# Kernel tuning notes

Hardware: AMD Instinct MI355X
Metric: run time of the kernel (lower is better)

Reference implementation:

```python
import jax, jax.numpy as jnp
import numpy as np

# --- dims (match init_kwargs) ---
H = 2048      # hidden_dim
NH = 16       # num_heads
QL = 1536     # q_latent_dim
KVL = 512     # kv_latent_dim
QR = 64       # q_rope_dim (== k_rope_dim)
QN = 128      # q_nope_dim
KR = 64       # k_rope_dim
KN = 128      # k_nope_dim
VD = 128      # v_dim
B, S = 1, 2048
BASE = 10000.0
EPS = 1e-6


def rms_norm(x, w, eps=EPS):
    xf = x.astype(jnp.float32)
    var = jnp.mean(xf * xf, axis=-1, keepdims=True)
    return w * (xf * jax.lax.rsqrt(var + eps)).astype(x.dtype)


def rope_cos_sin(seq_len, dim, base=BASE):
    inv_freq = 1.0 / (base ** (jnp.arange(0, dim, 2, dtype=jnp.float32) / dim))
    t = jnp.arange(seq_len, dtype=jnp.float32)
    freqs = jnp.outer(t, inv_freq)
    emb = jnp.concatenate([freqs, freqs], axis=-1)  # [S, dim]
    return jnp.cos(emb), jnp.sin(emb)


def rotate_half(x):
    d = x.shape[-1] // 2
    return jnp.concatenate([-x[..., d:], x[..., :d]], axis=-1)


def apply_rotary_pos_emb(q, k, cos, sin, position_ids):
    # cos/sin: [S, d]; position_ids: [B, S] -> [B, 1, S, d]
    cos = cos[position_ids][:, None]
    sin = sin[position_ids][:, None]

    def interleave(x):  # matches view(b,h,s,d//2,2).transpose(4,3).reshape
        b, h, s, d = x.shape
        return x.reshape(b, h, s, d // 2, 2).transpose(0, 1, 2, 4, 3).reshape(b, h, s, d)

    q = interleave(q)
    k = interleave(k)
    return q * cos + rotate_half(q) * sin, k * cos + rotate_half(k) * sin


def setup_inputs() -> dict:
    key = jax.random.key(0)
    ks = jax.random.split(key, 8)
    sc = 0.02
    hidden_states = jax.random.normal(ks[0], (B, S, H), dtype=jnp.float32)
    position_ids = jnp.broadcast_to(jnp.arange(S, dtype=jnp.int32), (B, S))
    attn_mask = jnp.tril(jnp.ones((S, S), dtype=jnp.int32))[None, None]  # causal, [1,1,S,S]
    return {
        "hidden_states": hidden_states,
        "position_ids": position_ids,
        "attn_mask": attn_mask,
        "q_down_w": jax.random.normal(ks[1], (QL, H), jnp.float32) * sc,
        "kv_down_w": jax.random.normal(ks[2], (KVL + KR, H), jnp.float32) * sc,
        "q_up_w": jax.random.normal(ks[3], (NH * (QN + QR), QL), jnp.float32) * sc,
        "k_up_w": jax.random.normal(ks[4], (NH * (KN + VD), KVL), jnp.float32) * sc,
        "o_w": jax.random.normal(ks[5], (H, NH * VD), jnp.float32) * sc,
        "q_norm_w": jnp.ones((QL,), jnp.float32),
        "kv_norm_w": jnp.ones((KVL + KR,), jnp.float32),
    }


def reference(hidden_states, position_ids, attn_mask, q_down_w, kv_down_w,
              q_up_w, k_up_w, o_w, q_norm_w, kv_norm_w):
    bsz, seq_len, _ = hidden_states.shape

    # --- query path: down-proj -> RMSNorm -> up-proj ---
    latent_cq = rms_norm(hidden_states @ q_down_w.T, q_norm_w)        # [B,S,QL]
    q = latent_cq @ q_up_w.T                                          # [B,S,NH*(QN+QR)]
    q = q.reshape(bsz, seq_len, NH, QN + QR).transpose(0, 2, 1, 3)    # [B,NH,S,QN+QR]
    q_nope, q_pe = q[..., :QN], q[..., QN:]

    # --- kv path: down-proj -> RMSNorm -> split latent / shared k_pe ---
    compressed_kv = rms_norm(hidden_states @ kv_down_w.T, kv_norm_w)  # [B,S,KVL+KR]
    latent_ckv, k_pe = compressed_kv[..., :KVL], compressed_kv[..., KVL:]
    kv = latent_ckv @ k_up_w.T                                        # [B,S,NH*(KN+VD)]
    kv = kv.reshape(bsz, seq_len, NH, KN + VD).transpose(0, 2, 1, 3)  # [B,NH,S,KN+VD]
    k_nope, value = kv[..., :KN], kv[..., KN:]

    # --- partial RoPE on rotary sub-dims ---
    cos, sin = rope_cos_sin(seq_len, QR)
    k_pe = k_pe[:, None]                                              # [B,1,S,KR] shared across heads
    q_rope, k_rope = apply_rotary_pos_emb(q_pe, k_pe, cos, sin, position_ids)
    k_rope = jnp.broadcast_to(k_rope, (bsz, NH, seq_len, KR))

    query = jnp.concatenate([q_rope, q_nope], axis=-1)                # [B,NH,S,QR+QN]
    key = jnp.concatenate([k_rope, k_nope], axis=-1)                  # [B,NH,S,KR+KN]

    # --- explicit attention (no 1/sqrt(d) scale, matching the source) ---
    attn_weights = jnp.einsum('bhqd,bhkd->bhqk', query, key)
    attn_weights = jnp.where(attn_mask == 0, -jnp.inf, attn_weights)
    attn_weights = jax.nn.softmax(attn_weights, axis=-1)
    attn_output = jnp.einsum('bhqk,bhkd->bhqd', attn_weights, value)
    attn_output = attn_output.transpose(0, 2, 1, 3).reshape(bsz, seq_len, NH * VD)
    attn_output = attn_output @ o_w.T                                 # [B,S,H]
    return attn_weights, attn_output
```

## Files before the change

kernel.cpp:

```cpp
#include <hip/hip_runtime.h>
#include <cstdint>
#include <cmath>

typedef _Float16 f16;
using f16x8 = __attribute__((ext_vector_type(8))) _Float16;
using f16x4 = __attribute__((ext_vector_type(4))) _Float16;
using f32x4 = __attribute__((ext_vector_type(4))) float;

#define NHEAD 16
#define SEQ   2048
#define KS    2
#define NEG_INF -3.0e38f

static __device__ __forceinline__ f32x4 mfma16(f16x8 a, f16x8 b, f32x4 c) {
    return __builtin_amdgcn_mfma_f32_16x16x32_f16(a, b, c, 0, 0, 0);
}

static __device__ __forceinline__ void gload16(const void* gp, void* lp) {
    __builtin_amdgcn_global_load_lds(
        (const __attribute__((address_space(1))) unsigned int*)gp,
        (__attribute__((address_space(3))) unsigned int*)lp, 16, 0, 0);
}

__global__ __launch_bounds__(256) void k_cvt_all(
    const float* __restrict__ hsrc, const float* __restrict__ qdw, const float* __restrict__ kvdw,
    const float* __restrict__ quw, const float* __restrict__ kuw, const float* __restrict__ ow,
    f16* __restrict__ h16, f16* __restrict__ dw16, f16* __restrict__ quw16,
    f16* __restrict__ kuw16, f16* __restrict__ ow16)
{
    constexpr int C1 = 1048576;
    constexpr int C2 = C1 + 786432;
    constexpr int C3 = C2 + 327680;
    constexpr int C4 = C3 + 1179648;
    constexpr int C5 = C4 + 524288;
    int chunk = blockIdx.x * 256 + threadIdx.x;
    const float* src; f16* dst; int off; int nvalid;
    if (chunk < C1)      { src = hsrc; dst = h16;  off = chunk;      nvalid = 4194304; }
    else if (chunk < C2) { src = qdw;  dst = dw16; off = chunk - C1; nvalid = 3145728; }
    else if (chunk < C3) { src = kvdw; dst = dw16 + 3145728; off = chunk - C2; nvalid = 1179648; }
    else if (chunk < C4) { src = quw;  dst = quw16; off = chunk - C3; nvalid = 4718592; }
    else if (chunk < C5) { src = kuw;  dst = kuw16; off = chunk - C4; nvalid = 2097152; }
    else                 { src = ow;   dst = ow16;  off = chunk - C5; nvalid = 4194304; }
    int i = off * 4;
    f16x4 o;
#pragma unroll
    for (int k = 0; k < 4; k++) {
        int idx = i + k;
        float v = (idx < nvalid) ? src[idx] : 0.f;
        o[k] = (f16)v;
    }
    *(f16x4*)&dst[i] = o;
}

__global__ __launch_bounds__(256) void k_rope_table(float* __restrict__ cs)
{
    int idx = blockIdx.x * 256 + threadIdx.x;
    int t = idx >> 5;
    int j = idx & 31;
    float invf = (float)pow(10000.0, -(double)j / 32.0);
    float ang  = (float)t * invf;
    cs[t * 64 + j]      = (float)cos((double)ang);
    cs[t * 64 + 32 + j] = (float)sin((double)ang);
}

template <typename OutT, bool NT>
static __device__ __forceinline__ void gemm_body(const f16* __restrict__ A, const f16* __restrict__ B,
                                                 OutT* __restrict__ C, int K, int ldc,
                                                 int m0, int n0, int k0, int k1,
                                                 f16* __restrict__ lds)
{
    const int tid  = threadIdx.x;
    const int lane = tid & 63;
    const int wv   = tid >> 6;
    const int l15  = lane & 15;
    const int lg   = lane >> 4;
    const int wm   = (wv >> 1) * 64;
    const int wn   = (wv & 1) * 64;

    f32x4 acc[4][4] = {};

    f16* As = lds;
    f16* Bs = lds + 8192;

    const int srow = tid >> 3;
    const int g    = (tid & 7) ^ (srow & 7);
    const f16* ap = &A[(size_t)(m0 + srow) * K + g * 8];
    const f16* bp = &B[(size_t)(n0 + srow) * K + g * 8];
    const int ldst = wv * 512;

    for (int kt = k0; kt < k1; kt += 64) {
        __syncthreads();
#pragma unroll
        for (int p = 0; p < 4; p++) {
            gload16(ap + (size_t)(p * 32) * K + kt, As + p * 2048 + ldst);
            gload16(bp + (size_t)(p * 32) * K + kt, Bs + p * 2048 + ldst);
        }
        __syncthreads();
#pragma unroll
        for (int ki = 0; ki < 2; ki++) {
            f16x8 af[4], bf[4];
#pragma unroll
            for (int i = 0; i < 4; i++) {
                const int ar = wm + i * 16 + l15;
                af[i] = *(const f16x8*)&As[ar * 64 + (((ki * 4 + lg) ^ (ar & 7)) << 3)];
            }
#pragma unroll
            for (int i = 0; i < 4; i++) {
                const int br = wn + i * 16 + l15;
                bf[i] = *(const f16x8*)&Bs[br * 64 + (((ki * 4 + lg) ^ (br & 7)) << 3)];
            }
#pragma unroll
            for (int i = 0; i < 4; i++)
#pragma unroll
                for (int j = 0; j < 4; j++)
                    acc[i][j] = mfma16(af[i], bf[j], acc[i][j]);
        }
    }
#pragma unroll
    for (int i = 0; i < 4; i++) {
#pragma unroll
        for (int j = 0; j < 4; j++) {
            const int row = m0 + wm + i * 16 + lg * 4;
            const int col = n0 + wn + j * 16 + l15;
#pragma unroll
            for (int r = 0; r < 4; r++) {
                if constexpr (NT)
                    __builtin_nontemporal_store((OutT)acc[i][j][r], &C[(size_t)(row + r) * ldc + col]);
                else
                    C[(size_t)(row + r) * ldc + col] = (OutT)acc[i][j][r];
            }
        }
    }
}

template <typename OutT, bool NT, int SPLITK>
__global__ __launch_bounds__(256) void k_gemm(const f16* __restrict__ A, const f16* __restrict__ B,
                                              OutT* __restrict__ C, int K, int ldc, size_t zstride)
{
    __shared__ __align__(16) f16 lds[16384];
    const int ks   = (SPLITK > 1) ? (int)blockIdx.z : 0;
    const int ksub = K / SPLITK;
    gemm_body<OutT, NT>(A, B, C + (size_t)ks * zstride, K, ldc,
                        blockIdx.y * 128, blockIdx.x * 128, ks * ksub, ks * ksub + ksub, lds);
}

__global__ __launch_bounds__(256) void k_up_fused(const f16* __restrict__ cq, const f16* __restrict__ quw,
                                                  f16* __restrict__ q_all,
                                                  const f16* __restrict__ lat, const f16* __restrict__ kuw,
                                                  f16* __restrict__ kv_all)
{
    __shared__ __align__(16) f16 lds[16384];
    if (blockIdx.x < 24)
        gemm_body<f16, false>(cq, quw, q_all, 1536, 3072,
                              blockIdx.y * 128, blockIdx.x * 128, 0, 1536, lds);
    else
        gemm_body<f16, false>(lat, kuw, kv_all, 512, 4096,
                              blockIdx.y * 128, (blockIdx.x - 24) * 128, 0, 512, lds);
}

__global__ __launch_bounds__(256) void k_add2f(const float* __restrict__ p, float* __restrict__ out)
{
    size_t i = ((size_t)blockIdx.x * 256 + threadIdx.x) * 4;
    f32x4 a = *(const f32x4*)&p[i];
    f32x4 b = *(const f32x4*)&p[(size_t)2048 * 2048 + i];
    __builtin_nontemporal_store(a + b, (f32x4*)&out[i]);
}

__global__ __launch_bounds__(256) void k_rms_both(const float* __restrict__ P0, const float* __restrict__ P1,
                                                  const float* __restrict__ wq, const float* __restrict__ wkv,
                                                  f16* __restrict__ cq, f16* __restrict__ lat,
                                                  f16* __restrict__ kro, const float* __restrict__ cs)
{
    const int row = blockIdx.x, tid = threadIdx.x;
    const float* a = &P0[(size_t)row * 2176];
    const float* b = &P1[(size_t)row * 2176];
    float ssq = 0.f, ssk = 0.f;
    for (int c = tid; c < 1536; c += 256) { float v = a[c] + b[c]; ssq += v * v; }
    for (int c = 1536 + tid; c < 2112; c += 256) { float v = a[c] + b[c]; ssk += v * v; }
#pragma unroll
    for (int off = 32; off > 0; off >>= 1) {
        ssq += __shfl_xor(ssq, off);
        ssk += __shfl_xor(ssk, off);
    }
    __shared__ float part[4][2];
    if ((tid & 63) == 0) { part[tid >> 6][0] = ssq; part[tid >> 6][1] = ssk; }
    __syncthreads();
    float totq = part[0][0] + part[1][0] + part[2][0] + part[3][0];
    float totk = part[0][1] + part[1][1] + part[2][1] + part[3][1];
    float scq = 1.f / sqrtf(totq / 1536.f + 1e-6f);
    float sck = 1.f / sqrtf(totk / 576.f + 1e-6f);
    for (int c = tid; c < 1536; c += 256)
        cq[(size_t)row * 1536 + c] = (f16)(wq[c] * (a[c] + b[c]) * scq);
    for (int c = tid; c < 512; c += 256)
        lat[(size_t)row * 512 + c] = (f16)(wkv[c] * (a[1536 + c] + b[1536 + c]) * sck);
    if (tid < 32) {
        int j = tid;
        float va = wkv[512 + 2 * j] * (a[2048 + 2 * j] + b[2048 + 2 * j]) * sck;
        float vb = wkv[512 + 2 * j + 1] * (a[2048 + 2 * j + 1] + b[2048 + 2 * j + 1]) * sck;
        float cv = cs[row * 64 + j], sv = cs[row * 64 + 32 + j];
        kro[row * 64 + j]      = (f16)(va * cv - vb * sv);
        kro[row * 64 + 32 + j] = (f16)(vb * cv + va * sv);
    }
}

__global__ __launch_bounds__(256) void k_asm_q(const f16* __restrict__ q_all, const float* __restrict__ cs,
                                               f16* __restrict__ Qf)
{
    size_t idx = (size_t)blockIdx.x * 256 + threadIdx.x;
    if (idx >= (size_t)16 * 2048 * 192) return;
    int d = (int)(idx % 192);
    size_t hs = idx / 192;
    int s = (int)(hs % 2048);
    int h = (int)(hs / 2048);
    const f16* qrow = &q_all[(size_t)s * 3072 + h * 192];
    float v;
    if (d < 64) {
        int j = d & 31;
        float a = (float)qrow[128 + 2 * j], b = (float)qrow[128 + 2 * j + 1];
        float cv = cs[s * 64 + j], sv = cs[s * 64 + 32 + j];
        v = (d < 32) ? (a * cv - b * sv) : (b * cv + a * sv);
    } else {
        v = (float)qrow[d - 64];
    }
    Qf[idx] = (f16)v;
}

__global__ __launch_bounds__(256) void k_asm_kv(const f16* __restrict__ kv_all,
                                                f16* __restrict__ Knope,
                                                f16* __restrict__ Vt)
{
    __shared__ __align__(16) f16 Vs[128][136];
    const int s0 = blockIdx.x * 128;
    const int h  = blockIdx.y;
    const int tid = threadIdx.x;

#pragma unroll
    for (int i = 0; i < 16; i++) {
        const int c = tid + 256 * i;
        const int s_loc = c >> 5;
        const int g = c & 31;
        f16x8 v = *(const f16x8*)&kv_all[(size_t)(s0 + s_loc) * 4096 + h * 256 + g * 8];
        if (g < 16) {
            *(f16x8*)&Knope[((size_t)h * 2048 + s0 + s_loc) * 128 + g * 8] = v;
        } else {
            const int d0 = (g - 16) * 8;
#pragma unroll
            for (int k = 0; k < 8; k++) Vs[d0 + k][s_loc] = v[k];
        }
    }
    __syncthreads();
#pragma unroll
    for (int i = 0; i < 8; i++) {
        const int c = tid + 256 * i;
        const int d = c >> 4;
        const int gs = c & 15;
        f16x8 v = *(const f16x8*)&Vs[d][gs * 8];
        *(f16x8*)&Vt[((size_t)h * 128 + d) * 2048 + s0 + gs * 8] = v;
    }
}

__global__ __launch_bounds__(256) void k_stats(
    const f16* __restrict__ Qf, const f16* __restrict__ Krope, const f16* __restrict__ Knope,
    float* __restrict__ mlpart)
{
    const int h  = blockIdx.z;
    const int ks = blockIdx.y;
    const int qt = blockIdx.x;
    const int q0 = qt * 64;
    const int tid = threadIdx.x;
    const int lane = tid & 63;
    const int wv = tid >> 6;
    const int l15 = lane & 15;
    const int lg  = lane >> 4;
    const int rowb = q0 + wv * 16;

    __shared__ __align__(16) f16 Ks_[64][200];

    f16x8 qf[6];
    {
        const f16* qbase = &Qf[((size_t)h * SEQ + rowb + l15) * 192];
#pragma unroll
        for (int kf = 0; kf < 6; kf++)
            qf[kf] = *(const f16x8*)&qbase[kf * 32 + lg * 8];
    }

    float m[4], l[4];
#pragma unroll
    for (int r = 0; r < 4; r++) { m[r] = NEG_INF; l[r] = 0.f; }

    const int srow = tid >> 2;
    const int sp4  = tid & 3;
    const f32x4 vzero = {0.f, 0.f, 0.f, 0.f};

    for (int t = ks; t <= qt; t += KS) {
        const int c0 = t * 64;
        __syncthreads();
#pragma unroll
        for (int i = 0; i < 6; i++) {
            const int p = sp4 + 4 * i;
            f16x8 v;
            if (p < 8) v = *(const f16x8*)&Krope[(size_t)(c0 + srow) * 64 + p * 8];
            else       v = *(const f16x8*)&Knope[((size_t)h * SEQ + c0 + srow) * 128 + (p - 8) * 8];
            *(f16x8*)&Ks_[srow][p * 8] = v;
        }
        __syncthreads();

        f32x4 s[4];
#pragma unroll
        for (int ni = 0; ni < 4; ni++) {
            s[ni] = vzero;
            const f16* kp = &Ks_[ni * 16 + l15][0];
#pragma unroll
            for (int kf = 0; kf < 6; kf++)
                s[ni] = mfma16(qf[kf], *(const f16x8*)&kp[kf * 32 + lg * 8], s[ni]);
        }

        float vmax[4] = {NEG_INF, NEG_INF, NEG_INF, NEG_INF};
#pragma unroll
        for (int ni = 0; ni < 4; ni++) {
            const int col = c0 + ni * 16 + l15;
#pragma unroll
            for (int r = 0; r < 4; r++) {
                const int row = rowb + lg * 4 + r;
                float v = (col <= row) ? s[ni][r] : NEG_INF;
                s[ni][r] = v;
                vmax[r] = fmaxf(vmax[r], v);
            }
        }
#pragma unroll
        for (int off = 1; off < 16; off <<= 1)
#pragma unroll
            for (int r = 0; r < 4; r++)
                vmax[r] = fmaxf(vmax[r], __shfl_xor(vmax[r], off));
#pragma unroll
        for (int r = 0; r < 4; r++) {
            const float nm = fmaxf(m[r], vmax[r]);
            float es = 0.f;
#pragma unroll
            for (int ni = 0; ni < 4; ni++) es += expf(s[ni][r] - nm);
#pragma unroll
            for (int off = 1; off < 16; off <<= 1) es += __shfl_xor(es, off);
            l[r] = l[r] * expf(m[r] - nm) + es;
            m[r] = nm;
        }
    }

    if (l15 == 0) {
#pragma unroll
        for (int r = 0; r < 4; r++) {
            const int rin = wv * 16 + lg * 4 + r;
            float* mp = &mlpart[((((size_t)h * 32 + qt) * KS + ks) * 64 + rin) * 2];
            mp[0] = m[r];
            mp[1] = l[r];
        }
    }
}

__global__ __launch_bounds__(256) void k_mlcomb(const float* __restrict__ mlpart,
                                                float* __restrict__ mlbuf)
{
    int idx = blockIdx.x * 256 + threadIdx.x;
    if (idx >= 16 * 2048) return;
    int h = idx >> 11, row = idx & 2047;
    int qt = row >> 6, rin = row & 63;
    float mm = NEG_INF;
    float mk[KS], lk[KS];
#pragma unroll
    for (int ks = 0; ks < KS; ks++) {
        const float* mp = &mlpart[((((size_t)h * 32 + qt) * KS + ks) * 64 + rin) * 2];
        mk[ks] = mp[0]; lk[ks] = mp[1];
        mm = fmaxf(mm, mk[ks]);
    }
    float ll = 0.f;
#pragma unroll
    for (int ks = 0; ks < KS; ks++) ll += lk[ks] * expf(mk[ks] - mm);
    mlbuf[(size_t)idx * 2]     = mm;
    mlbuf[(size_t)idx * 2 + 1] = 1.f / ll;
}

__global__ __launch_bounds__(256) void k_pv(
    const f16* __restrict__ Qf, const f16* __restrict__ Krope, const f16* __restrict__ Knope,
    const f16* __restrict__ Vt, const float* __restrict__ mlbuf,
    float* __restrict__ attnw,
    f16* __restrict__ Opart)
{
    const int h  = blockIdx.z;
    const int ks = blockIdx.y;
    const int qt = blockIdx.x;
    const int q0 = qt * 64;
    const int tid = threadIdx.x;
    const int lane = tid & 63;
    const int wv = tid >> 6;
    const int l15 = lane & 15;
    const int lg  = lane >> 4;
    const int rowb = q0 + wv * 16;

    __shared__ __align__(16) f16 Ks_[64][200];
    __shared__ __align__(16) f16 Vs[128][72];
    __shared__ __align__(16) f16 Plds[4][16][72];

    f16x8 qf[6];
    {
        const f16* qbase = &Qf[((size_t)h * SEQ + rowb + l15) * 192];
#pragma unroll
        for (int kf = 0; kf < 6; kf++)
            qf[kf] = *(const f16x8*)&qbase[kf * 32 + lg * 8];
    }

    float mr[4], rlr[4];
#pragma unroll
    for (int r = 0; r < 4; r++) {
        const int row = rowb + lg * 4 + r;
        mr[r]  = mlbuf[((size_t)h * SEQ + row) * 2];
        rlr[r] = mlbuf[((size_t)h * SEQ + row) * 2 + 1];
    }

    f32x4 o[8] = {};
    const f32x4 vzero = {0.f, 0.f, 0.f, 0.f};
    const int srow = tid >> 2;
    const int sp4  = tid & 3;

    for (int t = ks; t <= qt; t += KS) {
        const int c0 = t * 64;
        __syncthreads();
#pragma unroll
        for (int i = 0; i < 6; i++) {
            const int p = sp4 + 4 * i;
            f16x8 v;
            if (p < 8) v = *(const f16x8*)&Krope[(size_t)(c0 + srow) * 64 + p * 8];
            else       v = *(const f16x8*)&Knope[((size_t)h * SEQ + c0 + srow) * 128 + (p - 8) * 8];
            *(f16x8*)&Ks_[srow][p * 8] = v;
        }
#pragma unroll
        for (int i = 0; i < 4; i++) {
            const int c = tid + 256 * i;
            const int d = c >> 3, x = c & 7;
            *(f16x8*)&Vs[d][x * 8] = *(const f16x8*)&Vt[((size_t)h * 128 + d) * SEQ + c0 + x * 8];
        }
        __syncthreads();

        f32x4 s[4];
#pragma unroll
        for (int ni = 0; ni < 4; ni++) {
            s[ni] = vzero;
            const f16* kp = &Ks_[ni * 16 + l15][0];
#pragma unroll
            for (int kf = 0; kf < 6; kf++)
                s[ni] = mfma16(qf[kf], *(const f16x8*)&kp[kf * 32 + lg * 8], s[ni]);
        }

#pragma unroll
        for (int ni = 0; ni < 4; ni++) {
            const int col = c0 + ni * 16 + l15;
#pragma unroll
            for (int r = 0; r < 4; r++) {
                const int row = rowb + lg * 4 + r;
                float p = (col <= row) ? expf(s[ni][r] - mr[r]) * rlr[r] : 0.f;
                __builtin_nontemporal_store(p, &attnw[((size_t)h * SEQ + row) * SEQ + col]);
                Plds[wv][lg * 4 + r][ni * 16 + l15] = (f16)p;
            }
        }
        asm volatile("" ::: "memory");

        f16x8 pa0 = *(const f16x8*)&Plds[wv][l15][lg * 8];
        f16x8 pa1 = *(const f16x8*)&Plds[wv][l15][32 + lg * 8];
#pragma unroll
        for (int nd = 0; nd < 8; nd++) {
            const f16* vp = &Vs[nd * 16 + l15][lg * 8];
            o[nd] = mfma16(pa0, *(const f16x8*)&vp[0],  o[nd]);
            o[nd] = mfma16(pa1, *(const f16x8*)&vp[32], o[nd]);
        }
    }

#pragma unroll
    for (int nd = 0; nd < 8; nd++)
#pragma unroll
        for (int r = 0; r < 4; r++) {
            const int row = rowb + lg * 4 + r;
            Opart[((size_t)ks * SEQ + row) * 2048 + h * 128 + nd * 16 + l15] = (f16)o[nd][r];
        }

    if (ks == KS - 1) {
        const int cstart = q0 + 64;
        const int zc = SEQ - cstart;
        if (zc > 0) {
            const int nchunk = zc >> 2;
            for (int i = tid; i < 64 * nchunk; i += 256) {
                const int r  = i / nchunk;
                const int cc = (i - r * nchunk) << 2;
                __builtin_nontemporal_store(vzero,
                    (f32x4*)&attnw[((size_t)h * SEQ + q0 + r) * SEQ + cstart + cc]);
            }
        }
    }
}

__global__ __launch_bounds__(256) void k_ocomb(const f16* __restrict__ Opart, f16* __restrict__ Ohead)
{
    size_t i = ((size_t)blockIdx.x * 256 + threadIdx.x) * 8;
    f16x8 a = *(const f16x8*)&Opart[i];
    f16x8 b = *(const f16x8*)&Opart[(size_t)SEQ * 2048 + i];
    f16x8 o;
#pragma unroll
    for (int k = 0; k < 8; k++) o[k] = (f16)((float)a[k] + (float)b[k]);
    *(f16x8*)&Ohead[i] = o;
}

extern "C" void kernel_launch(void* const* d_in, const int* in_sizes, int n_in,
                              void* d_out, int out_size, void* d_ws, size_t ws_size,
                              hipStream_t stream)
{
    (void)in_sizes; (void)n_in; (void)out_size; (void)ws_size;
    const float* hidden    = (const float*)d_in[0];
    const float* q_down_w  = (const float*)d_in[3];
    const float* kv_down_w = (const float*)d_in[4];
    const float* q_up_w    = (const float*)d_in[5];
    const float* k_up_w    = (const float*)d_in[6];
    const float* o_w       = (const float*)d_in[7];
    const float* q_norm_w  = (const float*)d_in[8];
    const float* kv_norm_w = (const float*)d_in[9];

    float* attnw = (float*)d_out;
    float* outp  = attnw + (size_t)NHEAD * SEQ * SEQ;

    char* wp = (char*)d_ws;
    auto aws = [&](size_t bytes) { void* p = (void*)wp; wp += (bytes + 255) & ~(size_t)255; return p; };
    f16*  ow16  = (f16*)aws((size_t)2048 * 2048 * 2);
    f16*  Ohead = (f16*)aws((size_t)2048 * 2048 * 2);
    f16*  Qf    = (f16*)aws((size_t)16 * 2048 * 192 * 2);
    f16*  Knope = (f16*)aws((size_t)16 * 2048 * 128 * 2);
    f16*  Vt    = (f16*)aws((size_t)16 * 128 * 2048 * 2);
    f16*  Krope = (f16*)aws((size_t)2048 * 64 * 2);
    float* cs   = (float*)aws((size_t)2048 * 64 * 4);
    float* mlbuf  = (float*)aws((size_t)16 * 2048 * 2 * 4);
    float* mlpart = (float*)aws((size_t)16 * 32 * KS * 64 * 2 * 4);
    f16*  Opart   = (f16*)aws((size_t)KS * 2048 * 2048 * 2);
    float* opp    = (float*)Qf;

    char* sp = (char*)d_out;
    auto aso = [&](size_t bytes) { void* p = (void*)sp; sp += (bytes + 255) & ~(size_t)255; return p; };
    f16*  h16      = (f16*)aso((size_t)2048 * 2048 * 2);
    f16*  dw16     = (f16*)aso((size_t)2176 * 2048 * 2);
    f16*  quw16    = (f16*)aso((size_t)3072 * 1536 * 2);
    f16*  kuw16    = (f16*)aso((size_t)4096 * 512 * 2);
    float* down_part = (float*)aso((size_t)2 * 2048 * 2176 * 4);
    f16*  cq16     = (f16*)aso((size_t)2048 * 1536 * 2);
    f16*  latent16 = (f16*)aso((size_t)2048 * 512 * 2);
    f16*  q_all    = (f16*)aso((size_t)2048 * 3072 * 2);
    f16*  kv_all   = (f16*)aso((size_t)2048 * 4096 * 2);

    k_rope_table<<<dim3(256), dim3(256), 0, stream>>>(cs);

    k_cvt_all<<<dim3(19200), dim3(256), 0, stream>>>(
        hidden, q_down_w, kv_down_w, q_up_w, k_up_w, o_w,
        h16, dw16, quw16, kuw16, ow16);

    k_gemm<float, false, 2><<<dim3(17, 16, 2), dim3(256), 0, stream>>>(
        h16, dw16, down_part, 2048, 2176, (size_t)2048 * 2176);

    k_rms_both<<<dim3(2048), dim3(256), 0, stream>>>(
        down_part, down_part + (size_t)2048 * 2176, q_norm_w, kv_norm_w,
        cq16, latent16, Krope, cs);

    k_up_fused<<<dim3(56, 16), dim3(256), 0, stream>>>(cq16, quw16, q_all, latent16, kuw16, kv_all);

    k_asm_q<<<dim3((16 * 2048 * 192) / 256), dim3(256), 0, stream>>>(q_all, cs, Qf);
    k_asm_kv<<<dim3(16, 16), dim3(256), 0, stream>>>(kv_all, Knope, Vt);

    k_stats<<<dim3(32, KS, 16), dim3(256), 0, stream>>>(Qf, Krope, Knope, mlpart);
    k_mlcomb<<<dim3(128), dim3(256), 0, stream>>>(mlpart, mlbuf);
    k_pv<<<dim3(32, KS, 16), dim3(256), 0, stream>>>(Qf, Krope, Knope, Vt, mlbuf, attnw, Opart);
    k_ocomb<<<dim3(2048), dim3(256), 0, stream>>>(Opart, Ohead);

    k_gemm<float, false, 2><<<dim3(16, 16, 2), dim3(256), 0, stream>>>(
        Ohead, ow16, opp, 2048, 2048, (size_t)2048 * 2048);
    k_add2f<<<dim3(4096), dim3(256), 0, stream>>>(opp, outp);
}
```

Baseline: 376.2 us.

## Fuse small kernels, vectorize Q assembly, split stats over four key slices

Folds the rope table into the conversion kernel and merges the Q and KV assembly kernels into one launch. The Q assembly now writes 8 halves per thread instead of one element. The m/l combine kernel is dropped and its work moves into k_pv. k_stats now splits keys four ways instead of two for more parallelism. This trades fewer launches and better load balance for some redundant recombination work in every k_pv block.

```diff
diff --git a/kernel.cpp b/kernel.cpp
--- a/kernel.cpp
+++ b/kernel.cpp
@@ -10,6 +10,7 @@
 #define NHEAD 16
 #define SEQ   2048
 #define KS    2
+#define KSS   4
 #define NEG_INF -3.0e38f
 
 static __device__ __forceinline__ f32x4 mfma16(f16x8 a, f16x8 b, f32x4 c) {
@@ -26,14 +27,26 @@
     const float* __restrict__ hsrc, const float* __restrict__ qdw, const float* __restrict__ kvdw,
     const float* __restrict__ quw, const float* __restrict__ kuw, const float* __restrict__ ow,
     f16* __restrict__ h16, f16* __restrict__ dw16, f16* __restrict__ quw16,
-    f16* __restrict__ kuw16, f16* __restrict__ ow16)
+    f16* __restrict__ kuw16, f16* __restrict__ ow16, float* __restrict__ cs)
 {
     constexpr int C1 = 1048576;
     constexpr int C2 = C1 + 786432;
     constexpr int C3 = C2 + 327680;
     constexpr int C4 = C3 + 1179648;
     constexpr int C5 = C4 + 524288;
+    constexpr int C6 = C5 + 1048576;
     int chunk = blockIdx.x * 256 + threadIdx.x;
+    if (chunk >= C6) {
+        int idx = chunk - C6;
+        if (idx < 65536) {
+            int t = idx >> 5, j = idx & 31;
+            float invf = (float)pow(10000.0, -(double)j / 32.0);
+            float ang  = (float)t * invf;
+            cs[t * 64 + j]      = (float)cos((double)ang);
+            cs[t * 64 + 32 + j] = (float)sin((double)ang);
+        }
+        return;
+    }
     const float* src; f16* dst; int off; int nvalid;
     if (chunk < C1)      { src = hsrc; dst = h16;  off = chunk;      nvalid = 4194304; }
     else if (chunk < C2) { src = qdw;  dst = dw16; off = chunk - C1; nvalid = 3145728; }
@@ -50,17 +63,6 @@
         o[k] = (f16)v;
     }
     *(f16x4*)&dst[i] = o;
-}
-
-__global__ __launch_bounds__(256) void k_rope_table(float* __restrict__ cs)
-{
-    int idx = blockIdx.x * 256 + threadIdx.x;
-    int t = idx >> 5;
-    int j = idx & 31;
-    float invf = (float)pow(10000.0, -(double)j / 32.0);
-    float ang  = (float)t * invf;
-    cs[t * 64 + j]      = (float)cos((double)ang);
-    cs[t * 64 + 32 + j] = (float)sin((double)ang);
 }
 
 template <typename OutT, bool NT>
@@ -203,37 +205,44 @@
     }
 }
 
-__global__ __launch_bounds__(256) void k_asm_q(const f16* __restrict__ q_all, const float* __restrict__ cs,
-                                               f16* __restrict__ Qf)
-{
-    size_t idx = (size_t)blockIdx.x * 256 + threadIdx.x;
-    if (idx >= (size_t)16 * 2048 * 192) return;
-    int d = (int)(idx % 192);
-    size_t hs = idx / 192;
-    int s = (int)(hs % 2048);
-    int h = (int)(hs / 2048);
-    const f16* qrow = &q_all[(size_t)s * 3072 + h * 192];
-    float v;
-    if (d < 64) {
-        int j = d & 31;
-        float a = (float)qrow[128 + 2 * j], b = (float)qrow[128 + 2 * j + 1];
-        float cv = cs[s * 64 + j], sv = cs[s * 64 + 32 + j];
-        v = (d < 32) ? (a * cv - b * sv) : (b * cv + a * sv);
-    } else {
-        v = (float)qrow[d - 64];
-    }
-    Qf[idx] = (f16)v;
-}
-
-__global__ __launch_bounds__(256) void k_asm_kv(const f16* __restrict__ kv_all,
-                                                f16* __restrict__ Knope,
-                                                f16* __restrict__ Vt)
+__global__ __launch_bounds__(256) void k_asm_all(const f16* __restrict__ q_all, const float* __restrict__ cs,
+                                                 f16* __restrict__ Qf,
+                                                 const f16* __restrict__ kv_all,
+                                                 f16* __restrict__ Knope,
+                                                 f16* __restrict__ Vt)
 {
     __shared__ __align__(16) f16 Vs[128][136];
-    const int s0 = blockIdx.x * 128;
-    const int h  = blockIdx.y;
     const int tid = threadIdx.x;
 
+    if (blockIdx.x < 3072) {
+        const int gid = blockIdx.x * 256 + tid;
+        const int p   = gid % 24;
+        const int rowi = gid / 24;
+        const int h = rowi >> 11, s = rowi & 2047;
+        const f16* qrow = &q_all[(size_t)s * 3072 + h * 192];
+        f16x8 o;
+        if (p < 8) {
+            const int pp = (p < 4) ? p : (p - 4);
+            f16x8 la = *(const f16x8*)&qrow[128 + 16 * pp];
+            f16x8 lb = *(const f16x8*)&qrow[136 + 16 * pp];
+            const float* cb = &cs[s * 64 + 8 * pp];
+#pragma unroll
+            for (int e = 0; e < 8; e++) {
+                float av = (float)((e < 4) ? la[2 * e] : lb[2 * e - 8]);
+                float bv = (float)((e < 4) ? la[2 * e + 1] : lb[2 * e - 7]);
+                float cv = cb[e], sv = cb[32 + e];
+                o[e] = (f16)((p < 4) ? (av * cv - bv * sv) : (bv * cv + av * sv));
+            }
+        } else {
+            o = *(const f16x8*)&qrow[8 * p - 64];
+        }
+        *(f16x8*)&Qf[((size_t)h * SEQ + s) * 192 + 8 * p] = o;
+        return;
+    }
+
+    const int b  = blockIdx.x - 3072;
+    const int s0 = (b & 15) * 128;
+    const int h  = b >> 4;
 #pragma unroll
     for (int i = 0; i < 16; i++) {
         const int c = tid + 256 * i;
@@ -276,72 +285,73 @@
 
     __shared__ __align__(16) f16 Ks_[64][200];
 
-    f16x8 qf[6];
-    {
-        const f16* qbase = &Qf[((size_t)h * SEQ + rowb + l15) * 192];
-#pragma unroll
-        for (int kf = 0; kf < 6; kf++)
-            qf[kf] = *(const f16x8*)&qbase[kf * 32 + lg * 8];
-    }
-
     float m[4], l[4];
 #pragma unroll
     for (int r = 0; r < 4; r++) { m[r] = NEG_INF; l[r] = 0.f; }
 
-    const int srow = tid >> 2;
-    const int sp4  = tid & 3;
-    const f32x4 vzero = {0.f, 0.f, 0.f, 0.f};
-
-    for (int t = ks; t <= qt; t += KS) {
-        const int c0 = t * 64;
-        __syncthreads();
-#pragma unroll
-        for (int i = 0; i < 6; i++) {
-            const int p = sp4 + 4 * i;
-            f16x8 v;
-            if (p < 8) v = *(const f16x8*)&Krope[(size_t)(c0 + srow) * 64 + p * 8];
-            else       v = *(const f16x8*)&Knope[((size_t)h * SEQ + c0 + srow) * 128 + (p - 8) * 8];
-            *(f16x8*)&Ks_[srow][p * 8] = v;
-        }
-        __syncthreads();
-
-        f32x4 s[4];
-#pragma unroll
-        for (int ni = 0; ni < 4; ni++) {
-            s[ni] = vzero;
-            const f16* kp = &Ks_[ni * 16 + l15][0];
+    if (ks <= qt) {
+        f16x8 qf[6];
+        {
+            const f16* qbase = &Qf[((size_t)h * SEQ + rowb + l15) * 192];
 #pragma unroll
             for (int kf = 0; kf < 6; kf++)
-                s[ni] = mfma16(qf[kf], *(const f16x8*)&kp[kf * 32 + lg * 8], s[ni]);
-        }
-
-        float vmax[4] = {NEG_INF, NEG_INF, NEG_INF, NEG_INF};
-#pragma unroll
-        for (int ni = 0; ni < 4; ni++) {
-            const int col = c0 + ni * 16 + l15;
+                qf[kf] = *(const f16x8*)&qbase[kf * 32 + lg * 8];
+        }
+        const int srow = tid >> 2;
+        const int sp4  = tid & 3;
+        const f32x4 vzero = {0.f, 0.f, 0.f, 0.f};
+
+        for (int t = ks; t <= qt; t += KSS) {
+            const int c0 = t * 64;
+            __syncthreads();
+#pragma unroll
+            for (int i = 0; i < 6; i++) {
+                const int p = sp4 + 4 * i;
+                f16x8 v;
+                if (p < 8) v = *(const f16x8*)&Krope[(size_t)(c0 + srow) * 64 + p * 8];
+                else       v = *(const f16x8*)&Knope[((size_t)h * SEQ + c0 + srow) * 128 + (p - 8) * 8];
+                *(f16x8*)&Ks_[srow][p * 8] = v;
+            }
+            __syncthreads();
+
+            f32x4 s[4];
+#pragma unroll
+            for (int ni = 0; ni < 4; ni++) {
+                s[ni] = vzero;
+                const f16* kp = &Ks_[ni * 16 + l15][0];
+#pragma unroll
+                for (int kf = 0; kf < 6; kf++)
+                    s[ni] = mfma16(qf[kf], *(const f16x8*)&kp[kf * 32 + lg * 8], s[ni]);
+            }
+
+            float vmax[4] = {NEG_INF, NEG_INF, NEG_INF, NEG_INF};
+#pragma unroll
+            for (int ni = 0; ni < 4; ni++) {
+                const int col = c0 + ni * 16 + l15;
+#pragma unroll
+                for (int r = 0; r < 4; r++) {
+                    const int row = rowb + lg * 4 + r;
+                    float v = (col <= row) ? s[ni][r] : NEG_INF;
+                    s[ni][r] = v;
+                    vmax[r] = fmaxf(vmax[r], v);
+                }
+            }
+#pragma unroll
+            for (int off = 1; off < 16; off <<= 1)
+#pragma unroll
+                for (int r = 0; r < 4; r++)
+                    vmax[r] = fmaxf(vmax[r], __shfl_xor(vmax[r], off));
 #pragma unroll
             for (int r = 0; r < 4; r++) {
-                const int row = rowb + lg * 4 + r;
-                float v = (col <= row) ? s[ni][r] : NEG_INF;
-                s[ni][r] = v;
-                vmax[r] = fmaxf(vmax[r], v);
-            }
-        }
-#pragma unroll
-        for (int off = 1; off < 16; off <<= 1)
-#pragma unroll
-            for (int r = 0; r < 4; r++)
-                vmax[r] = fmaxf(vmax[r], __shfl_xor(vmax[r], off));
-#pragma unroll
-        for (int r = 0; r < 4; r++) {
-            const float nm = fmaxf(m[r], vmax[r]);
-            float es = 0.f;
-#pragma unroll
-            for (int ni = 0; ni < 4; ni++) es += expf(s[ni][r] - nm);
-#pragma unroll
-            for (int off = 1; off < 16; off <<= 1) es += __shfl_xor(es, off);
-            l[r] = l[r] * expf(m[r] - nm) + es;
-            m[r] = nm;
+                const float nm = fmaxf(m[r], vmax[r]);
+                float es = 0.f;
+#pragma unroll
+                for (int ni = 0; ni < 4; ni++) es += expf(s[ni][r] - nm);
+#pragma unroll
+                for (int off = 1; off < 16; off <<= 1) es += __shfl_xor(es, off);
+                l[r] = l[r] * expf(m[r] - nm) + es;
+                m[r] = nm;
+            }
         }
     }
 
@@ -349,38 +359,16 @@
 #pragma unroll
         for (int r = 0; r < 4; r++) {
             const int rin = wv * 16 + lg * 4 + r;
-            float* mp = &mlpart[((((size_t)h * 32 + qt) * KS + ks) * 64 + rin) * 2];
+            float* mp = &mlpart[((((size_t)h * 32 + qt) * KSS + ks) * 64 + rin) * 2];
             mp[0] = m[r];
             mp[1] = l[r];
         }
     }
 }
 
-__global__ __launch_bounds__(256) void k_mlcomb(const float* __restrict__ mlpart,
-                                                float* __restrict__ mlbuf)
-{
-    int idx = blockIdx.x * 256 + threadIdx.x;
-    if (idx >= 16 * 2048) return;
-    int h = idx >> 11, row = idx & 2047;
-    int qt = row >> 6, rin = row & 63;
-    float mm = NEG_INF;
-    float mk[KS], lk[KS];
-#pragma unroll
-    for (int ks = 0; ks < KS; ks++) {
-        const float* mp = &mlpart[((((size_t)h * 32 + qt) * KS + ks) * 64 + rin) * 2];
-        mk[ks] = mp[0]; lk[ks] = mp[1];
-        mm = fmaxf(mm, mk[ks]);
-    }
-    float ll = 0.f;
-#pragma unroll
-    for (int ks = 0; ks < KS; ks++) ll += lk[ks] * expf(mk[ks] - mm);
-    mlbuf[(size_t)idx * 2]     = mm;
-    mlbuf[(size_t)idx * 2 + 1] = 1.f / ll;
-}
-
 __global__ __launch_bounds__(256) void k_pv(
     const f16* __restrict__ Qf, const f16* __restrict__ Krope, const f16* __restrict__ Knope,
-    const f16* __restrict__ Vt, const float* __restrict__ mlbuf,
+    const f16* __restrict__ Vt, const float* __restrict__ mlpart,
     float* __restrict__ attnw,
     f16* __restrict__ Opart)
 {
@@ -408,11 +396,24 @@
     }
 
     float mr[4], rlr[4];
-#pragma unroll
-    for (int r = 0; r < 4; r++) {
-        const int row = rowb + lg * 4 + r;
-        mr[r]  = mlbuf[((size_t)h * SEQ + row) * 2];
-        rlr[r] = mlbuf[((size_t)h * SEQ + row) * 2 + 1];
+    {
+        const float* base = &mlpart[(((size_t)h * 32 + qt) * KSS) * 64 * 2];
+#pragma unroll
+        for (int r = 0; r < 4; r++) {
+            const int rin = wv * 16 + lg * 4 + r;
+            float mm = NEG_INF, mk[KSS], lk[KSS];
+#pragma unroll
+            for (int k2 = 0; k2 < KSS; k2++) {
+                mk[k2] = base[(k2 * 64 + rin) * 2];
+                lk[k2] = base[(k2 * 64 + rin) * 2 + 1];
+                mm = fmaxf(mm, mk[k2]);
+            }
+            float ll = 0.f;
+#pragma unroll
+            for (int k2 = 0; k2 < KSS; k2++) ll += lk[k2] * expf(mk[k2] - mm);
+            mr[r]  = mm;
+            rlr[r] = 1.f / ll;
+        }
     }
 
     f32x4 o[8] = {};
@@ -532,8 +533,7 @@
     f16*  Vt    = (f16*)aws((size_t)16 * 128 * 2048 * 2);
     f16*  Krope = (f16*)aws((size_t)2048 * 64 * 2);
     float* cs   = (float*)aws((size_t)2048 * 64 * 4);
-    float* mlbuf  = (float*)aws((size_t)16 * 2048 * 2 * 4);
-    float* mlpart = (float*)aws((size_t)16 * 32 * KS * 64 * 2 * 4);
+    float* mlpart = (float*)aws((size_t)16 * 32 * KSS * 64 * 2 * 4);
     f16*  Opart   = (f16*)aws((size_t)KS * 2048 * 2048 * 2);
     float* opp    = (float*)Qf;
 
@@ -549,11 +549,9 @@
     f16*  q_all    = (f16*)aso((size_t)2048 * 3072 * 2);
     f16*  kv_all   = (f16*)aso((size_t)2048 * 4096 * 2);
 
-    k_rope_table<<<dim3(256), dim3(256), 0, stream>>>(cs);
-
-    k_cvt_all<<<dim3(19200), dim3(256), 0, stream>>>(
+    k_cvt_all<<<dim3(19456), dim3(256), 0, stream>>>(
         hidden, q_down_w, kv_down_w, q_up_w, k_up_w, o_w,
-        h16, dw16, quw16, kuw16, ow16);
+        h16, dw16, quw16, kuw16, ow16, cs);
 
     k_gemm<float, false, 2><<<dim3(17, 16, 2), dim3(256), 0, stream>>>(
         h16, dw16, down_part, 2048, 2176, (size_t)2048 * 2176);
@@ -564,12 +562,10 @@
 
     k_up_fused<<<dim3(56, 16), dim3(256), 0, stream>>>(cq16, quw16, q_all, latent16, kuw16, kv_all);
 
-    k_asm_q<<<dim3((16 * 2048 * 192) / 256), dim3(256), 0, stream>>>(q_all, cs, Qf);
-    k_asm_kv<<<dim3(16, 16), dim3(256), 0, stream>>>(kv_all, Knope, Vt);
-
-    k_stats<<<dim3(32, KS, 16), dim3(256), 0, stream>>>(Qf, Krope, Knope, mlpart);
-    k_mlcomb<<<dim3(128), dim3(256), 0, stream>>>(mlpart, mlbuf);
-    k_pv<<<dim3(32, KS, 16), dim3(256), 0, stream>>>(Qf, Krope, Knope, Vt, mlbuf, attnw, Opart);
+    k_asm_all<<<dim3(3072 + 256), dim3(256), 0, stream>>>(q_all, cs, Qf, kv_all, Knope, Vt);
+
+    k_stats<<<dim3(32, KSS, 16), dim3(256), 0, stream>>>(Qf, Krope, Knope, mlpart);
+    k_pv<<<dim3(32, KS, 16), dim3(256), 0, stream>>>(Qf, Krope, Knope, Vt, mlpart, attnw, Opart);
     k_ocomb<<<dim3(2048), dim3(256), 0, stream>>>(Opart, Ohead);
 
     k_gemm<float, false, 2><<<dim3(16, 16, 2), dim3(256), 0, stream>>>(
```

Result: no change. 376.7 us (+0.1%).
